# Kernel optimization log

Hardware: AMD Instinct MI355X
Metric: run time of the kernel (lower is better)

Reference implementation:

```python
import jax, jax.numpy as jnp
import numpy as np

H = 1024      # embe_size / hidden size
L = 2         # layer_num
LBL = 5       # label_size
B, S = 64, 512


def setup_inputs() -> dict:
    key = jax.random.key(0)
    ks = jax.random.split(key, 7)
    sc = 1.0 / np.sqrt(H)
    inputs = jax.random.normal(ks[0], (B, S, H), dtype=jnp.float32)
    Wx = jax.random.uniform(ks[1], (L, H, 4 * H), minval=-sc, maxval=sc, dtype=jnp.float32)
    bx = jax.random.uniform(ks[2], (L, 4 * H), minval=-sc, maxval=sc, dtype=jnp.float32)
    Wh = jax.random.uniform(ks[3], (L, H, 4 * H), minval=-sc, maxval=sc, dtype=jnp.float32)
    bh = jax.random.uniform(ks[4], (L, 4 * H), minval=-sc, maxval=sc, dtype=jnp.float32)
    scp = 1.0 / np.sqrt(H)
    Wp = jax.random.uniform(ks[5], (H, LBL), minval=-scp, maxval=scp, dtype=jnp.float32)
    bp = jax.random.uniform(ks[6], (LBL,), minval=-scp, maxval=scp, dtype=jnp.float32)
    return {"inputs": inputs, "Wx": Wx, "bx": bx, "Wh": Wh, "bh": bh, "Wp": Wp, "bp": bp}


def _lstm_forward(inputs, Wx, bx, Wh, bh, Wp, bp):
    # inputs: [B,S,H] -> time-major [S,B,H]
    x = jnp.transpose(inputs, (1, 0, 2))
    n_layers = Wx.shape[0]
    bsz, hid = x.shape[1], Wx.shape[1]
    for l in range(n_layers):
        Wh_l, bh_l = Wh[l], bh[l]
        # precompute input->gate projection for all timesteps: [S,B,4H]
        xg = jnp.einsum('sbh,hg->sbg', x, Wx[l]) + bx[l]

        def step(carry, xg_t):
            h, c = carry
            feat = xg_t + h @ Wh_l + bh_l
            i, f, g, o = jnp.split(feat, 4, axis=-1)
            c = jax.nn.sigmoid(f) * c + jax.nn.sigmoid(i) * jnp.tanh(g)
            h = jnp.tanh(c) * jax.nn.sigmoid(o)
            return (h, c), h

        h0 = jnp.zeros((bsz, hid), dtype=x.dtype)
        _, x = jax.lax.scan(step, (h0, h0), xg)
        # dropout is identity at inference (eval mode)
    # max-pool over time (max_pool1d over full seq), then classify
    pooled = jnp.max(x, axis=0)  # [B,H]
    return pooled @ Wp + bp      # [B,label_size]


def reference(inputs, Wx, bx, Wh, bh, Wp, bp):
    return _lstm_forward(inputs, Wx, bx, Wh, bh, Wp, bp)
```

## Files before the change

kernel.cpp:

```cpp
#include <hip/hip_runtime.h>
#include <hip/hip_bf16.h>

typedef _Float16 half8 __attribute__((ext_vector_type(8)));
typedef _Float16 half4v __attribute__((ext_vector_type(4)));
typedef float f32x4 __attribute__((ext_vector_type(4)));

#define BB 64
#define SS 512
#define HH 1024
#define G4 4096
#define NSTEP 514

#define BAR_GLB 256
#define BAR_GO  288

__device__ __forceinline__ float sigmf(float x) { return 1.0f / (1.0f + __expf(-x)); }
__device__ __forceinline__ float tanhfast(float x) { return 2.0f / (1.0f + __expf(-2.0f * x)) - 1.0f; }

__global__ __launch_bounds__(256) void convert_x_kernel(const float* __restrict__ in,
                                                        _Float16* __restrict__ x16) {
  size_t idx = (size_t)blockIdx.x * 256 + threadIdx.x;
  int h4 = (int)(idx & 255);
  int s  = (int)((idx >> 8) & 511);
  int b  = (int)(idx >> 17);
  const float4* src = (const float4*)in;
  float4 v = src[((size_t)b * SS + s) * 256 + h4];
  half4v hv = { (_Float16)v.x, (_Float16)v.y, (_Float16)v.z, (_Float16)v.w };
  *(half4v*)(x16 + ((size_t)s * BB + b) * HH + (size_t)h4 * 4) = hv;
}

__global__ __launch_bounds__(256) void convert_w_kernel(const float* __restrict__ Wx,
                                                        const float* __restrict__ Wh,
                                                        _Float16* __restrict__ wT) {
  __shared__ float tile[32][33];
  int m = blockIdx.x >> 12;
  int t = blockIdx.x & 4095;
  int tn = t & 127, tk = t >> 7;
  int l = m & 1, which = m >> 1;
  const float* src = (which ? Wh : Wx) + (size_t)l * HH * G4;
  int tx = threadIdx.x & 31, ty = threadIdx.x >> 5;
#pragma unroll
  for (int p = 0; p < 4; ++p) {
    int k = tk * 32 + ty + 8 * p, n = tn * 32 + tx;
    tile[ty + 8 * p][tx] = src[(size_t)k * G4 + n];
  }
  __syncthreads();
  _Float16* dst = wT + (size_t)m * G4 * HH;
#pragma unroll
  for (int p = 0; p < 4; ++p) {
    int n = tn * 32 + ty + 8 * p, k = tk * 32 + tx;
    dst[(size_t)n * HH + k] = (_Float16)tile[tx][ty + 8 * p];
  }
}

__global__ __launch_bounds__(512, 2) void lstm_persist(
    const _Float16* __restrict__ x16, const _Float16* __restrict__ wT,
    const float* __restrict__ bx, const float* __restrict__ bh,
    _Float16* __restrict__ h1buf, _Float16* __restrict__ h2buf,
    float* __restrict__ hmax, unsigned int* __restrict__ bar) {
  __shared__ float part[8][32][72];
  __shared__ float red[64][37];

  const int bid = blockIdx.x;
  const int layer = bid >> 7;
  const int j = bid & 127;
  const int tid = threadIdx.x;
  const int w = tid >> 6, l = tid & 63;
  const int l15 = l & 15, lg = l >> 4;
  const int grp = bid & 7;

  const _Float16* wTe = wT + (size_t)layer * G4 * HH;
  const _Float16* wTr = wT + (size_t)(2 + layer) * G4 * HH;
  const int kbase = w * 128;
  half8 Be[8], Br[8];
#pragma unroll
  for (int kk = 0; kk < 4; ++kk)
#pragma unroll
    for (int c = 0; c < 2; ++c) {
      int nl = 16 * c + l15;
      size_t gcol = (size_t)((nl & 3) * HH + 8 * j + (nl >> 2));
      Be[kk * 2 + c] = *(const half8*)(wTe + gcol * HH + kbase + 32 * kk + 8 * lg);
      Br[kk * 2 + c] = *(const half8*)(wTr + gcol * HH + kbase + 32 * kk + 8 * lg);
    }

  const int erow = tid >> 2, m2 = tid & 3;
  const int hc0 = 8 * j + 2 * m2;
  float bs[8];
  float c0 = 0.f, c1 = 0.f, hm0 = -2.f, hm1 = -2.f;
  if (tid < 256) {
#pragma unroll
    for (int dm = 0; dm < 2; ++dm)
#pragma unroll
      for (int g = 0; g < 4; ++g)
        bs[4 * dm + g] = bx[layer * G4 + g * HH + hc0 + dm] + bh[layer * G4 + g * HH + hc0 + dm];
  }

#pragma unroll 1
  for (int t = 0; t < NSTEP; ++t) {
    const bool act = (layer == 0) ? (t < SS) : (t >= 2);
    f32x4 acc[8];
#pragma unroll
    for (int i = 0; i < 8; ++i) acc[i] = (f32x4){0.f, 0.f, 0.f, 0.f};

    if (act) {
      const _Float16* Ae = (layer == 0) ? x16 + (size_t)t * BB * HH
                                        : h1buf + (size_t)((t - 2) & 3) * BB * HH;
      const _Float16* aep = Ae + (size_t)l15 * HH + kbase + 8 * lg;
      half8 a[16];
#pragma unroll
      for (int rf = 0; rf < 4; ++rf)
#pragma unroll
        for (int kk = 0; kk < 4; ++kk)
          a[rf * 4 + kk] = *(const half8*)(aep + (size_t)(16 * rf) * HH + 32 * kk);
#pragma unroll
      for (int rf = 0; rf < 4; ++rf)
#pragma unroll
        for (int kk = 0; kk < 4; ++kk) {
          acc[rf * 2 + 0] = __builtin_amdgcn_mfma_f32_16x16x32_f16(a[rf * 4 + kk], Be[kk * 2 + 0], acc[rf * 2 + 0], 0, 0, 0);
          acc[rf * 2 + 1] = __builtin_amdgcn_mfma_f32_16x16x32_f16(a[rf * 4 + kk], Be[kk * 2 + 1], acc[rf * 2 + 1], 0, 0, 0);
        }
    }

    if (tid == 0) {
      while (__hip_atomic_load(bar + BAR_GO + 32 * grp, __ATOMIC_RELAXED,
                               __HIP_MEMORY_SCOPE_AGENT) < (unsigned)t)
        __builtin_amdgcn_s_sleep(1);
      __builtin_amdgcn_fence(__ATOMIC_ACQUIRE, "agent");
    }
    __syncthreads();

    if (act) {
      const _Float16* Ah = (layer == 0) ? h1buf + (size_t)((t - 1) & 3) * BB * HH
                                        : h2buf + (size_t)((t - 1) & 1) * BB * HH;
      const _Float16* ahp = Ah + (size_t)l15 * HH + kbase + 8 * lg;
      half8 a[16];
#pragma unroll
      for (int rf = 0; rf < 4; ++rf)
#pragma unroll
        for (int kk = 0; kk < 4; ++kk)
          a[rf * 4 + kk] = *(const half8*)(ahp + (size_t)(16 * rf) * HH + 32 * kk);
#pragma unroll
      for (int rf = 0; rf < 4; ++rf)
#pragma unroll
        for (int kk = 0; kk < 4; ++kk) {
          acc[rf * 2 + 0] = __builtin_amdgcn_mfma_f32_16x16x32_f16(a[rf * 4 + kk], Br[kk * 2 + 0], acc[rf * 2 + 0], 0, 0, 0);
          acc[rf * 2 + 1] = __builtin_amdgcn_mfma_f32_16x16x32_f16(a[rf * 4 + kk], Br[kk * 2 + 1], acc[rf * 2 + 1], 0, 0, 0);
        }

#pragma unroll
      for (int rf = 0; rf < 4; ++rf)
#pragma unroll
        for (int c = 0; c < 2; ++c)
          *(f32x4*)&part[w][16 * c + l15][16 * rf + 4 * lg] = acc[rf * 2 + c];
      __syncthreads();

      {
        int col = tid >> 4, rq = tid & 15;
        f32x4 s = {0.f, 0.f, 0.f, 0.f};
#pragma unroll
        for (int ww = 0; ww < 8; ++ww)
          s += *(const f32x4*)&part[ww][col][4 * rq];
        red[4 * rq + 0][col] = s[0];
        red[4 * rq + 1][col] = s[1];
        red[4 * rq + 2][col] = s[2];
        red[4 * rq + 3][col] = s[3];
      }
      __syncthreads();

      if (tid < 256) {
        float v[8];
#pragma unroll
        for (int q = 0; q < 8; ++q) v[q] = red[erow][8 * m2 + q] + bs[q];
        float i0 = sigmf(v[0]), f0 = sigmf(v[1]), g0 = tanhfast(v[2]), o0 = sigmf(v[3]);
        float i1 = sigmf(v[4]), f1 = sigmf(v[5]), g1 = tanhfast(v[6]), o1 = sigmf(v[7]);
        c0 = f0 * c0 + i0 * g0;
        c1 = f1 * c1 + i1 * g1;
        float h0 = tanhfast(c0) * o0;
        float h1 = tanhfast(c1) * o1;
        if (layer == 1) { hm0 = fmaxf(hm0, h0); hm1 = fmaxf(hm1, h1); }
        _Float16* hout = (layer == 0) ? h1buf + (size_t)(t & 3) * BB * HH
                                      : h2buf + (size_t)(t & 1) * BB * HH;
        unsigned int pk = ((unsigned int)__builtin_bit_cast(unsigned short, (_Float16)h1) << 16) |
                          (unsigned int)__builtin_bit_cast(unsigned short, (_Float16)h0);
        __hip_atomic_store((unsigned int*)hout + ((erow * HH + hc0) >> 1), pk,
                           __ATOMIC_RELAXED, __HIP_MEMORY_SCOPE_AGENT);
      }
    }

    __syncthreads();
    if (tid == 0) {
      unsigned prev = __hip_atomic_fetch_add(bar + 32 * grp, 1u, __ATOMIC_RELAXED,
                                             __HIP_MEMORY_SCOPE_AGENT);
      if (prev == 32u * (unsigned)(t + 1) - 1u) {
        unsigned p2 = __hip_atomic_fetch_add(bar + BAR_GLB, 1u, __ATOMIC_RELAXED,
                                             __HIP_MEMORY_SCOPE_AGENT);
        if (p2 == 8u * (unsigned)(t + 1) - 1u) {
#pragma unroll
          for (int gg = 0; gg < 8; ++gg)
            __hip_atomic_store(bar + BAR_GO + 32 * gg, (unsigned)(t + 1),
                               __ATOMIC_RELAXED, __HIP_MEMORY_SCOPE_AGENT);
        }
      }
    }
  }

  if (layer == 1 && tid < 256) {
    hmax[erow * HH + hc0]     = hm0;
    hmax[erow * HH + hc0 + 1] = hm1;
  }
}

__global__ __launch_bounds__(320) void classify_kernel(const float* __restrict__ hmax,
                                                       const float* __restrict__ Wp,
                                                       const float* __restrict__ bp,
                                                       float* __restrict__ out) {
  int tid = threadIdx.x;
  int b = tid / 5, jj = tid % 5;
  float s = bp[jj];
  const float* hp = hmax + (size_t)b * HH;
  for (int h = 0; h < HH; ++h) s = fmaf(hp[h], Wp[h * 5 + jj], s);
  out[tid] = s;
}

extern "C" void kernel_launch(void* const* d_in, const int* in_sizes, int n_in,
                              void* d_out, int out_size, void* d_ws, size_t ws_size,
                              hipStream_t stream) {
  const float* inputs = (const float*)d_in[0];
  const float* Wx = (const float*)d_in[1];
  const float* bx = (const float*)d_in[2];
  const float* Wh = (const float*)d_in[3];
  const float* bh = (const float*)d_in[4];
  const float* Wp = (const float*)d_in[5];
  const float* bp = (const float*)d_in[6];
  float* out = (float*)d_out;

  char* ws = (char*)d_ws;
  _Float16* x16   = (_Float16*)(ws + 0);
  _Float16* wT    = (_Float16*)(ws + 67108864);
  _Float16* h1buf = (_Float16*)(ws + 100663296);
  _Float16* h2buf = (_Float16*)(ws + 101187584);
  float*    hmax  = (float*)(ws + 101449728);
  unsigned int* bar = (unsigned int*)(ws + 101711872);

  hipMemsetAsync(h1buf, 0, 524288, stream);
  hipMemsetAsync(h2buf, 0, 262144, stream);
  hipMemsetAsync(bar, 0, 4096, stream);

  convert_x_kernel<<<32768, 256, 0, stream>>>(inputs, x16);
  convert_w_kernel<<<16384, 256, 0, stream>>>(Wx, Wh, wT);
  lstm_persist<<<256, 512, 0, stream>>>(x16, wT, bx, bh, h1buf, h2buf, hmax, bar);
  classify_kernel<<<1, 320, 0, stream>>>(hmax, Wp, bp, out);
}
```

Baseline: 5.195 ms.

## Decouple layer barriers using full h trajectory buffers instead of ring buffers

Replaces the single global barrier shared by both LSTM layers with separate per-layer barriers. Each layer now writes its hidden state for every timestep into a full-length trajectory buffer, so layer 1 only waits for layer 0's step t-1 rather than lock-stepping with it. This lets layer 0 run ahead and shortens each barrier to half the blocks. The cost is about 130MB of extra workspace, with a fallback to the old ring-buffer path when the workspace is too small. The acquire fence on the trajectory path is dropped, which may weaken memory ordering.

Measured after the change: 4.822 ms. 7.2% less time.

```diff
diff --git a/kernel.cpp b/kernel.cpp
--- a/kernel.cpp
+++ b/kernel.cpp
@@ -10,12 +10,30 @@
 #define HH 1024
 #define G4 4096
 #define NSTEP 514
-
-#define BAR_GLB 256
-#define BAR_GO  288
+#define SLOT 65536
+
+#define SB_ARR(g) ((g) * 32)
+#define SB_GLB 256
+#define SB_GO(g) (288 + (g) * 32)
+#define FB_ARR(L, g) ((L) * 256 + (g) * 32)
+#define FB_GLB(L) (512 + (L) * 32)
+#define FB_GO(L, g) (576 + (L) * 256 + (g) * 32)
 
 __device__ __forceinline__ float sigmf(float x) { return 1.0f / (1.0f + __expf(-x)); }
 __device__ __forceinline__ float tanhfast(float x) { return 2.0f / (1.0f + __expf(-2.0f * x)) - 1.0f; }
+
+__device__ __forceinline__ unsigned aload(const unsigned* p) {
+  return __hip_atomic_load(p, __ATOMIC_RELAXED, __HIP_MEMORY_SCOPE_AGENT);
+}
+__device__ __forceinline__ void wait_ge(const unsigned* p, unsigned tgt) {
+  while (aload(p) < tgt) __builtin_amdgcn_s_sleep(1);
+}
+__device__ __forceinline__ unsigned aadd(unsigned* p) {
+  return __hip_atomic_fetch_add(p, 1u, __ATOMIC_RELAXED, __HIP_MEMORY_SCOPE_AGENT);
+}
+__device__ __forceinline__ void astore(unsigned* p, unsigned v) {
+  __hip_atomic_store(p, v, __ATOMIC_RELAXED, __HIP_MEMORY_SCOPE_AGENT);
+}
 
 __global__ __launch_bounds__(256) void convert_x_kernel(const float* __restrict__ in,
                                                         _Float16* __restrict__ x16) {
@@ -53,11 +71,12 @@
   }
 }
 
+template <bool TRAJ>
 __global__ __launch_bounds__(512, 2) void lstm_persist(
     const _Float16* __restrict__ x16, const _Float16* __restrict__ wT,
     const float* __restrict__ bx, const float* __restrict__ bh,
     _Float16* __restrict__ h1buf, _Float16* __restrict__ h2buf,
-    float* __restrict__ hmax, unsigned int* __restrict__ bar) {
+    float* __restrict__ hmax, unsigned* __restrict__ bar) {
   __shared__ float part[8][32][72];
   __shared__ float red[64][37];
 
@@ -95,16 +114,26 @@
         bs[4 * dm + g] = bx[layer * G4 + g * HH + hc0 + dm] + bh[layer * G4 + g * HH + hc0 + dm];
   }
 
+  const int tmax = TRAJ ? (layer ? NSTEP : SS) : NSTEP;
+
 #pragma unroll 1
-  for (int t = 0; t < NSTEP; ++t) {
+  for (int t = 0; t < tmax; ++t) {
     const bool act = (layer == 0) ? (t < SS) : (t >= 2);
     f32x4 acc[8];
 #pragma unroll
     for (int i = 0; i < 8; ++i) acc[i] = (f32x4){0.f, 0.f, 0.f, 0.f};
 
     if (act) {
-      const _Float16* Ae = (layer == 0) ? x16 + (size_t)t * BB * HH
-                                        : h1buf + (size_t)((t - 2) & 3) * BB * HH;
+      const _Float16* Ae;
+      if (layer == 0) {
+        Ae = x16 + (size_t)t * SLOT;
+      } else if (TRAJ) {
+        if (tid == 0) wait_ge(bar + FB_GO(0, grp), (unsigned)(t - 1));
+        __syncthreads();
+        Ae = h1buf + (size_t)(t - 1) * SLOT;
+      } else {
+        Ae = h1buf + (size_t)((t - 2) & 3) * SLOT;
+      }
       const _Float16* aep = Ae + (size_t)l15 * HH + kbase + 8 * lg;
       half8 a[16];
 #pragma unroll
@@ -122,16 +151,23 @@
     }
 
     if (tid == 0) {
-      while (__hip_atomic_load(bar + BAR_GO + 32 * grp, __ATOMIC_RELAXED,
-                               __HIP_MEMORY_SCOPE_AGENT) < (unsigned)t)
-        __builtin_amdgcn_s_sleep(1);
-      __builtin_amdgcn_fence(__ATOMIC_ACQUIRE, "agent");
+      if (TRAJ) {
+        wait_ge(bar + FB_GO(layer, grp), (unsigned)t);
+      } else {
+        wait_ge(bar + SB_GO(grp), (unsigned)t);
+        __builtin_amdgcn_fence(__ATOMIC_ACQUIRE, "agent");
+      }
     }
     __syncthreads();
 
     if (act) {
-      const _Float16* Ah = (layer == 0) ? h1buf + (size_t)((t - 1) & 3) * BB * HH
-                                        : h2buf + (size_t)((t - 1) & 1) * BB * HH;
+      const _Float16* Ah;
+      if (layer == 0)
+        Ah = TRAJ ? h1buf + (size_t)t * SLOT
+                  : h1buf + (size_t)((t - 1) & 3) * SLOT;
+      else
+        Ah = TRAJ ? h2buf + (size_t)(t - 2) * SLOT
+                  : h2buf + (size_t)((t - 1) & 1) * SLOT;
       const _Float16* ahp = Ah + (size_t)l15 * HH + kbase + 8 * lg;
       half8 a[16];
 #pragma unroll
@@ -178,27 +214,38 @@
         float h0 = tanhfast(c0) * o0;
         float h1 = tanhfast(c1) * o1;
         if (layer == 1) { hm0 = fmaxf(hm0, h0); hm1 = fmaxf(hm1, h1); }
-        _Float16* hout = (layer == 0) ? h1buf + (size_t)(t & 3) * BB * HH
-                                      : h2buf + (size_t)(t & 1) * BB * HH;
-        unsigned int pk = ((unsigned int)__builtin_bit_cast(unsigned short, (_Float16)h1) << 16) |
-                          (unsigned int)__builtin_bit_cast(unsigned short, (_Float16)h0);
-        __hip_atomic_store((unsigned int*)hout + ((erow * HH + hc0) >> 1), pk,
-                           __ATOMIC_RELAXED, __HIP_MEMORY_SCOPE_AGENT);
+        _Float16* hout;
+        if (layer == 0)
+          hout = TRAJ ? h1buf + (size_t)(t + 1) * SLOT : h1buf + (size_t)(t & 3) * SLOT;
+        else
+          hout = TRAJ ? h2buf + (size_t)(t - 1) * SLOT : h2buf + (size_t)(t & 1) * SLOT;
+        unsigned pk = ((unsigned)__builtin_bit_cast(unsigned short, (_Float16)h1) << 16) |
+                      (unsigned)__builtin_bit_cast(unsigned short, (_Float16)h0);
+        astore((unsigned*)hout + ((erow * HH + hc0) >> 1), pk);
       }
     }
 
     __syncthreads();
     if (tid == 0) {
-      unsigned prev = __hip_atomic_fetch_add(bar + 32 * grp, 1u, __ATOMIC_RELAXED,
-                                             __HIP_MEMORY_SCOPE_AGENT);
-      if (prev == 32u * (unsigned)(t + 1) - 1u) {
-        unsigned p2 = __hip_atomic_fetch_add(bar + BAR_GLB, 1u, __ATOMIC_RELAXED,
-                                             __HIP_MEMORY_SCOPE_AGENT);
-        if (p2 == 8u * (unsigned)(t + 1) - 1u) {
-#pragma unroll
-          for (int gg = 0; gg < 8; ++gg)
-            __hip_atomic_store(bar + BAR_GO + 32 * gg, (unsigned)(t + 1),
-                               __ATOMIC_RELAXED, __HIP_MEMORY_SCOPE_AGENT);
+      if (TRAJ) {
+        unsigned prev = aadd(bar + FB_ARR(layer, grp));
+        if (prev == 16u * (unsigned)(t + 1) - 1u) {
+          unsigned p2 = aadd(bar + FB_GLB(layer));
+          if (p2 == 8u * (unsigned)(t + 1) - 1u) {
+#pragma unroll
+            for (int gg = 0; gg < 8; ++gg)
+              astore(bar + FB_GO(layer, gg), (unsigned)(t + 1));
+          }
+        }
+      } else {
+        unsigned prev = aadd(bar + SB_ARR(grp));
+        if (prev == 32u * (unsigned)(t + 1) - 1u) {
+          unsigned p2 = aadd(bar + SB_GLB);
+          if (p2 == 8u * (unsigned)(t + 1) - 1u) {
+#pragma unroll
+            for (int gg = 0; gg < 8; ++gg)
+              astore(bar + SB_GO(gg), (unsigned)(t + 1));
+          }
         }
       }
     }
@@ -235,19 +282,35 @@
   float* out = (float*)d_out;
 
   char* ws = (char*)d_ws;
-  _Float16* x16   = (_Float16*)(ws + 0);
-  _Float16* wT    = (_Float16*)(ws + 67108864);
-  _Float16* h1buf = (_Float16*)(ws + 100663296);
-  _Float16* h2buf = (_Float16*)(ws + 101187584);
-  float*    hmax  = (float*)(ws + 101449728);
-  unsigned int* bar = (unsigned int*)(ws + 101711872);
-
-  hipMemsetAsync(h1buf, 0, 524288, stream);
-  hipMemsetAsync(h2buf, 0, 262144, stream);
-  hipMemsetAsync(bar, 0, 4096, stream);
+  _Float16* x16 = (_Float16*)(ws + 0);
+  _Float16* wT  = (_Float16*)(ws + 67108864);
+
+  const size_t TRAJ_BYTES = (size_t)513 * 131072;
+  const size_t NEED_FAST = 100663296ull + 2 * TRAJ_BYTES + 262144 + 8192;
+  bool fast = ws_size >= NEED_FAST;
 
   convert_x_kernel<<<32768, 256, 0, stream>>>(inputs, x16);
   convert_w_kernel<<<16384, 256, 0, stream>>>(Wx, Wh, wT);
-  lstm_persist<<<256, 512, 0, stream>>>(x16, wT, bx, bh, h1buf, h2buf, hmax, bar);
-  classify_kernel<<<1, 320, 0, stream>>>(hmax, Wp, bp, out);
-}
+
+  if (fast) {
+    _Float16* h1traj = (_Float16*)(ws + 100663296);
+    _Float16* h2traj = (_Float16*)(ws + 100663296 + TRAJ_BYTES);
+    float* hmax = (float*)(ws + 100663296 + 2 * TRAJ_BYTES);
+    unsigned* bar = (unsigned*)(ws + 100663296 + 2 * TRAJ_BYTES + 262144);
+    hipMemsetAsync(h1traj, 0, 131072, stream);
+    hipMemsetAsync(h2traj, 0, 131072, stream);
+    hipMemsetAsync(bar, 0, 8192, stream);
+    lstm_persist<true><<<256, 512, 0, stream>>>(x16, wT, bx, bh, h1traj, h2traj, hmax, bar);
+    classify_kernel<<<1, 320, 0, stream>>>(hmax, Wp, bp, out);
+  } else {
+    _Float16* h1buf = (_Float16*)(ws + 100663296);
+    _Float16* h2buf = (_Float16*)(ws + 101187584);
+    float* hmax = (float*)(ws + 101449728);
+    unsigned* bar = (unsigned*)(ws + 101711872);
+    hipMemsetAsync(h1buf, 0, 524288, stream);
+    hipMemsetAsync(h2buf, 0, 262144, stream);
+    hipMemsetAsync(bar, 0, 8192, stream);
+    lstm_persist<false><<<256, 512, 0, stream>>>(x16, wT, bx, bh, h1buf, h2buf, hmax, bar);
+    classify_kernel<<<1, 320, 0, stream>>>(hmax, Wp, bp, out);
+  }
+}
```
